# Kernel tuning notes

Measured on AMD Instinct MI355X. Metric: run time of the kernel, lower is better.

The kernel has to match this reference:

```python
import jax, jax.numpy as jnp
import numpy as np

H, NH, HD = 1024, 16, 64
WIN = 256
W = WIN // 2  # one-sided window
EXP = 4
PAD_VAL = 0.0  # pad_token_id
B, S0 = 2, 2048
NEG = float(np.finfo(np.float32).min)


def setup_inputs() -> dict:
    key = jax.random.key(0)
    ks = jax.random.split(key, 12)

    def lin(k, fi, fo):
        k1, k2 = jax.random.split(k)
        w = jax.random.normal(k1, (fi, fo), jnp.float32) / np.float32(np.sqrt(fi))
        b = jax.random.normal(k2, (fo,), jnp.float32) * 0.02
        return w, b

    x = jax.random.normal(ks[0], (B, S0, H), jnp.float32)
    mask = jnp.zeros((B, S0), jnp.int32)  # 0 = real token, 1 = pad
    wq, bq = lin(ks[1], H, H)
    wk, bk = lin(ks[2], H, H)
    wv, bv = lin(ks[3], H, H)
    wqg, bqg = lin(ks[4], H, H)
    wkg, bkg = lin(ks[5], H, H)
    wvg, bvg = lin(ks[6], H, H)
    ln_g = jnp.ones((H,), jnp.float32)
    ln_b = jnp.zeros((H,), jnp.float32)
    w1, b1 = lin(ks[7], H, H * EXP)
    w2, b2 = lin(ks[8], H * EXP, H)
    return dict(x=x, mask=mask, wq=wq, bq=bq, wk=wk, bk=bk, wv=wv, bv=bv,
                wqg=wqg, bqg=bqg, wkg=wkg, bkg=bkg, wvg=wvg, bvg=bvg,
                ln_g=ln_g, ln_b=ln_b, w1=w1, b1=b1, w2=w2, b2=b2)


def _forward(x, mask, wq, bq, wk, bk, wv, bv, wqg, bqg, wkg, bkg, wvg, bvg,
             ln_g, ln_b, w1, b1, w2, b2):
    Bsz, s0, _ = x.shape
    pad = WIN - s0 % WIN
    xp = jnp.pad(x, ((0, 0), (0, pad), (0, 0)), constant_values=PAD_VAL)
    m = jnp.pad(mask, ((0, 0), (0, pad)), constant_values=1)
    S = s0 + pad
    lm = (m * -10000).at[:, -1].set(10000)  # [B,S]; task='cls': last token global
    is_masked = lm < 0
    remove = lm != 0  # masked OR global keys removed from local windows

    inv_sqrt = np.float32(1.0 / np.sqrt(HD))
    q = ((xp @ wq + bq) * inv_sqrt).reshape(Bsz, S, NH, HD)
    k = (xp @ wk + bk).reshape(Bsz, S, NH, HD)
    v = (xp @ wv + bv).reshape(Bsz, S, NH, HD)

    nc = S // W
    # chunked banded scores: query chunk of W attends to 3W keys (prev/self/next)
    qc = q.transpose(0, 2, 1, 3).reshape(Bsz, NH, nc, W, HD)
    kpad = jnp.pad(k.transpose(0, 2, 1, 3), ((0, 0), (0, 0), (W, W), (0, 0)))
    idx3w = jnp.arange(nc)[:, None] * W + jnp.arange(3 * W)[None, :]  # [nc,3W]
    kc = kpad[:, :, idx3w]  # [B,NH,nc,3W,HD]
    sc = jnp.einsum('bhcpd,bhckd->bhcpk', qc, kc)  # [B,NH,nc,W,3W]
    p_idx = jnp.arange(W)[:, None]
    d_idx = jnp.arange(2 * W + 1)[None, :]
    band = sc[:, :, :, p_idx, p_idx + d_idx]  # [B,NH,nc,W,2W+1]
    band = band.reshape(Bsz, NH, S, 2 * W + 1).transpose(0, 2, 1, 3)  # [B,S,NH,2W+1]

    # key index j = i + d - W for offset d in [0, 2W]
    j = jnp.arange(S)[:, None] + jnp.arange(2 * W + 1)[None, :] - W
    in_range = (j >= 0) & (j < S)
    jc = jnp.clip(j, 0, S - 1)
    fmask = jnp.where(remove, NEG, 0.0)  # [B,S]
    band = band + fmask[:, jc][:, :, None, :]
    band = jnp.where(in_range[None, :, None, :], band, -jnp.inf)

    # global key column (single global token = last position), concatenated in front
    gcol = jnp.einsum('bshd,bhd->bsh', q, k[:, -1])[..., None]  # [B,S,NH,1]
    scores = jnp.concatenate([gcol, band], axis=-1)  # [B,S,NH,2W+2]
    probs = jax.nn.softmax(scores, axis=-1)
    probs = jnp.where(is_masked[:, :, None, None], 0.0, probs)

    out_g = probs[..., 0][..., None] * v[:, -1][:, None]  # [B,S,NH,HD]
    lp = probs[..., 1:].transpose(0, 2, 1, 3).reshape(Bsz, NH, nc, W, 2 * W + 1)
    pc = jnp.zeros((Bsz, NH, nc, W, 3 * W), probs.dtype).at[:, :, :, p_idx, p_idx + d_idx].set(lp)
    vpad = jnp.pad(v.transpose(0, 2, 1, 3), ((0, 0), (0, 0), (W, W), (0, 0)))
    vc = vpad[:, :, idx3w]  # [B,NH,nc,3W,HD]
    out_l = jnp.einsum('bhcpk,bhckd->bhcpd', pc, vc).reshape(Bsz, NH, S, HD).transpose(0, 2, 1, 3)
    attn = (out_l + out_g).reshape(Bsz, S, H)

    # full global attention for the global token (separate projections)
    qg = ((xp[:, -1] @ wqg + bqg) * inv_sqrt).reshape(Bsz, NH, HD)
    kg = (xp @ wkg + bkg).reshape(Bsz, S, NH, HD)
    vg = (xp @ wvg + bvg).reshape(Bsz, S, NH, HD)
    gs = jnp.einsum('bhd,bshd->bhs', qg, kg)
    gs = jnp.where(is_masked[:, None, :], NEG, gs)
    gout = jnp.einsum('bhs,bshd->bhd', jax.nn.softmax(gs, axis=-1), vg).reshape(Bsz, H)
    attn = attn.at[:, -1].set(gout)

    y = (xp + attn)[:, :s0]  # residual then strip padding
    mu = y.mean(-1, keepdims=True)
    var = ((y - mu) ** 2).mean(-1, keepdims=True)
    y = (y - mu) * jax.lax.rsqrt(var + 1e-5) * ln_g + ln_b
    h = jax.nn.gelu(y @ w1 + b1, approximate=False)
    return y + (h @ w2 + b2)


def reference(x, mask, wq, bq, wk, bk, wv, bv, wqg, bqg, wkg, bkg, wvg, bvg,
              ln_g, ln_b, w1, b1, w2, b2):
    return _forward(x, mask, wq, bq, wk, bk, wv, bv, wqg, bqg, wkg, bkg,
                    wvg, bvg, ln_g, ln_b, w1, b1, w2, b2)
```

## Files before the change

kernel.cpp:

```cpp
#include <hip/hip_runtime.h>


using bf16x8 = __attribute__((ext_vector_type(8))) short;
using bf16x4 = __attribute__((ext_vector_type(4))) short;
using f32x4  = __attribute__((ext_vector_type(4))) float;

__device__ __forceinline__ float b2f(short s) {
    return __uint_as_float(((unsigned int)(unsigned short)s) << 16);
}
__device__ __forceinline__ short f2b(float f) {
    unsigned int u = __float_as_uint(f);
    u += 0x7fffu + ((u >> 16) & 1u);
    return (short)(u >> 16);
}
__device__ __forceinline__ f32x4 mfma16(bf16x8 a, bf16x8 b, f32x4 c) {
    return __builtin_amdgcn_mfma_f32_16x16x32_bf16(a, b, c, 0, 0, 0);
}
__device__ __forceinline__ float safe_exp(float x) {
    return expf((x <= 0.f) ? x : 0.f);
}
__device__ __forceinline__ void load_lds16(const short* g, short* l) {
    __builtin_amdgcn_global_load_lds((const __attribute__((address_space(1))) void*)g,
                                     (__attribute__((address_space(3))) void*)l, 16, 0, 0);
}
#define NEGF (-3.0e38f)

__global__ void cvt_f32_bf16(const float* __restrict__ in, short* __restrict__ out, int n) {
    int i = (blockIdx.x * 256 + threadIdx.x) * 4;
    f32x4 v = *(const f32x4*)(in + i);
    bf16x4 o;
#pragma unroll
    for (int j = 0; j < 4; ++j) o[j] = f2b(v[j]);
    *(bf16x4*)(out + i) = o;
}

__global__ void cvt_transpose(const float* __restrict__ in, short* __restrict__ out,
                              int R, int C) {
    __shared__ short tile[32][33];
    int bx = blockIdx.x * 32, by = blockIdx.y * 32;
    int tx = threadIdx.x, ty = threadIdx.y;
    for (int i = ty; i < 32; i += 8)
        tile[i][tx] = f2b(in[(size_t)(by + i) * C + bx + tx]);
    __syncthreads();
    for (int i = ty; i < 32; i += 8)
        out[(size_t)(bx + i) * R + by + tx] = tile[tx][i];
}

__global__ void cvt_transpose_qkv(const float* __restrict__ wq, const float* __restrict__ wk,
                                  const float* __restrict__ wv, short* __restrict__ out) {
    __shared__ short tile[32][33];
    const float* in = (blockIdx.z == 0) ? wq : (blockIdx.z == 1) ? wk : wv;
    short* dst = out + (size_t)blockIdx.z * 1024 * 1024;
    int bx = blockIdx.x * 32, by = blockIdx.y * 32;
    int tx = threadIdx.x, ty = threadIdx.y;
    for (int i = ty; i < 32; i += 8)
        tile[i][tx] = f2b(in[(size_t)(by + i) * 1024 + bx + tx]);
    __syncthreads();
    for (int i = ty; i < 32; i += 8)
        dst[(size_t)(bx + i) * 1024 + by + tx] = tile[tx][i];
}

__global__ void transpose_v(const short* __restrict__ QKV, short* __restrict__ Vt) {
    __shared__ short tile[32][33];
    int bh = blockIdx.z; int b = bh >> 4, h = bh & 15;
    int j0 = blockIdx.x * 32, d0 = blockIdx.y * 32;
    int tx = threadIdx.x, ty = threadIdx.y;
    const short* src = QKV + (size_t)b * 2048 * 3072 + 2048 + h * 64;
    for (int i = ty; i < 32; i += 8)
        tile[i][tx] = src[(size_t)(j0 + i) * 3072 + d0 + tx];
    __syncthreads();
    short* dst = Vt + ((size_t)bh * 64 + d0) * 2048 + j0;
    for (int i = ty; i < 32; i += 8)
        dst[(size_t)i * 2048 + tx] = tile[tx][i];
}

__global__ __launch_bounds__(256, 2) void gemm_bt(
    const short* __restrict__ A, const short* __restrict__ Bt,
    const float* __restrict__ bias0, const float* __restrict__ bias1,
    const float* __restrict__ bias2,
    short* __restrict__ C,
    int M, int N, int K, float scale, int scale_cols, int mode)
{
    __shared__ short As[128 * 32];
    __shared__ short Bs[128 * 32];
    int m0 = blockIdx.x * 128, n0 = blockIdx.y * 128;
    int t = threadIdx.x;
    int wave = t >> 6, lane = t & 63, quad = lane >> 4, l16 = lane & 15;
    int wr = (wave >> 1) * 64, wc = (wave & 1) * 64;

    int ch0 = wave * 64 + lane;
    int ch1 = (4 + wave) * 64 + lane;
    int r0 = ch0 >> 2, kc0 = (ch0 & 3) * 8;
    int r1 = ch1 >> 2, kc1 = (ch1 & 3) * 8;
    const short* a0 = A  + (size_t)(m0 + r0) * K + kc0;
    const short* a1 = A  + (size_t)(m0 + r1) * K + kc1;
    const short* b0 = Bt + (size_t)(n0 + r0) * K + kc0;
    const short* b1 = Bt + (size_t)(n0 + r1) * K + kc1;
    short* lA0 = As + wave * 512;
    short* lA1 = As + (4 + wave) * 512;
    short* lB0 = Bs + wave * 512;
    short* lB1 = Bs + (4 + wave) * 512;

    f32x4 acc[4][4] = {};
    for (int k0 = 0; k0 < K; k0 += 32) {
        load_lds16(a0 + k0, lA0);
        load_lds16(a1 + k0, lA1);
        load_lds16(b0 + k0, lB0);
        load_lds16(b1 + k0, lB1);
        __syncthreads();
        bf16x8 af[4], bfr[4];
#pragma unroll
        for (int i = 0; i < 4; ++i)
            af[i] = *(bf16x8*)(As + (wr + i * 16 + l16) * 32 + quad * 8);
#pragma unroll
        for (int j = 0; j < 4; ++j)
            bfr[j] = *(bf16x8*)(Bs + (wc + j * 16 + l16) * 32 + quad * 8);
#pragma unroll
        for (int i = 0; i < 4; ++i)
#pragma unroll
            for (int j = 0; j < 4; ++j)
                acc[i][j] = mfma16(af[i], bfr[j], acc[i][j]);
        __syncthreads();
    }
#pragma unroll
    for (int j = 0; j < 4; ++j) {
        int col = n0 + wc + j * 16 + l16;
        int seg = col >> 10;
        const float* bp = (seg == 0) ? bias0 : (seg == 1) ? bias1 : bias2;
        float bs = bp[col & 1023];
        float sc = (col < scale_cols) ? scale : 1.0f;
#pragma unroll
        for (int i = 0; i < 4; ++i) {
#pragma unroll
            for (int r = 0; r < 4; ++r) {
                int row = m0 + wr + i * 16 + quad * 4 + r;
                float v = acc[i][j][r] + bs;
                if (mode == 0) {
                    C[(size_t)row * N + col] = f2b(v * sc);
                } else {
                    v = 0.5f * v * (1.0f + erff(v * 0.70710678118f));
                    C[(size_t)row * N + col] = f2b(v);
                }
            }
        }
    }
}

__global__ __launch_bounds__(256, 4) void gemm64_bt(
    const short* __restrict__ A, const short* __restrict__ Bt,
    const float* __restrict__ bias, const float* __restrict__ resf,
    float* __restrict__ Cf, int M, int N, int K)
{
    __shared__ short As[64 * 32];
    __shared__ short Bs[64 * 32];
    int m0 = blockIdx.x * 64, n0 = blockIdx.y * 64;
    int t = threadIdx.x;
    int wave = t >> 6, lane = t & 63, quad = lane >> 4, l16 = lane & 15;
    int wr = (wave >> 1) * 32, wc = (wave & 1) * 32;

    int ch = wave * 64 + lane;
    int r0 = ch >> 2, kc0 = (ch & 3) * 8;
    const short* a0 = A  + (size_t)(m0 + r0) * K + kc0;
    const short* b0 = Bt + (size_t)(n0 + r0) * K + kc0;
    short* lA = As + wave * 512;
    short* lB = Bs + wave * 512;

    f32x4 acc[2][2] = {};
    for (int k0 = 0; k0 < K; k0 += 32) {
        load_lds16(a0 + k0, lA);
        load_lds16(b0 + k0, lB);
        __syncthreads();
        bf16x8 af[2], bfr[2];
#pragma unroll
        for (int i = 0; i < 2; ++i)
            af[i] = *(bf16x8*)(As + (wr + i * 16 + l16) * 32 + quad * 8);
#pragma unroll
        for (int j = 0; j < 2; ++j)
            bfr[j] = *(bf16x8*)(Bs + (wc + j * 16 + l16) * 32 + quad * 8);
#pragma unroll
        for (int i = 0; i < 2; ++i)
#pragma unroll
            for (int j = 0; j < 2; ++j)
                acc[i][j] = mfma16(af[i], bfr[j], acc[i][j]);
        __syncthreads();
    }
#pragma unroll
    for (int j = 0; j < 2; ++j) {
        int col = n0 + wc + j * 16 + l16;
        float bs = bias[col];
#pragma unroll
        for (int i = 0; i < 2; ++i) {
#pragma unroll
            for (int r = 0; r < 4; ++r) {
                int row = m0 + wr + i * 16 + quad * 4 + r;
                Cf[(size_t)row * N + col] = acc[i][j][r] + bs + resf[(size_t)row * N + col];
            }
        }
    }
}

__global__ __launch_bounds__(256, 2) void attn_kernel(
    const short* __restrict__ QKV, const short* __restrict__ Vt,
    const int* __restrict__ mask,
    const float* __restrict__ bk, const float* __restrict__ bv,
    short* __restrict__ attn)
{
    extern __shared__ char smem[];
    short* PsQ = (short*)smem;
    short* KV  = (short*)(smem + 34816);
    float* gkf = (float*)(smem + 53248);
    float* gvf = (float*)(smem + 53504);

    int blk = blockIdx.x;
    int c = blk & 15, h = (blk >> 4) & 15, b = blk >> 8;
    int t = threadIdx.x;
    int wave = t >> 6, lane = t & 63, quad = lane >> 4, l16 = lane & 15;
    int q0 = c * 128;
    const int bs_off = b * 2048;
    const short* Q = QKV + h * 64;
    const short* K = QKV + 1024 + h * 64;

#pragma unroll
    for (int l = 0; l < 4; ++l) {
        int idx = l * 256 + t;
        int p = idx >> 3, dc = (idx & 7) * 8;
        *(bf16x8*)(PsQ + p * 72 + dc) =
            *(const bf16x8*)(Q + ((size_t)(bs_off + q0 + p)) * 3072 + dc);
    }
    if (t < 64) { gkf[t] = bk[h * 64 + t]; gvf[t] = bv[h * 64 + t]; }
    __syncthreads();

    bf16x8 aq[2][2];
#pragma unroll
    for (int ti = 0; ti < 2; ++ti)
#pragma unroll
        for (int ks = 0; ks < 2; ++ks)
            aq[ti][ks] = *(bf16x8*)(PsQ + (wave * 32 + ti * 16 + l16) * 72 + ks * 32 + quad * 8);

    float s_g[2][4];
#pragma unroll
    for (int ti = 0; ti < 2; ++ti)
#pragma unroll
        for (int r = 0; r < 4; ++r) {
            int row = wave * 32 + ti * 16 + quad * 4 + r;
            float part = 0.f;
#pragma unroll
            for (int dd = 0; dd < 4; ++dd) {
                int d = l16 * 4 + dd;
                part += b2f(PsQ[row * 72 + d]) * gkf[d];
            }
#pragma unroll
            for (int dsh = 1; dsh < 16; dsh <<= 1) part += __shfl_xor(part, dsh);
            s_g[ti][r] = part;
        }

    f32x4 o_acc[2][4] = {};
    float m_run[2][4], l_run[2][4];
#pragma unroll
    for (int ti = 0; ti < 2; ++ti)
#pragma unroll
        for (int r = 0; r < 4; ++r) { m_run[ti][r] = NEGF; l_run[ti][r] = 0.f; }

    int kt_beg = (q0 == 0) ? 1 : 0;
    int kt_end = (q0 + 256 > 2048) ? 2 : 3;
    for (int kt = kt_beg; kt < kt_end; ++kt) {
        int jb = q0 + (kt - 1) * 128;
        __syncthreads();
#pragma unroll
        for (int l = 0; l < 4; ++l) {
            int idx = l * 256 + t;
            int p = idx >> 3, dc = (idx & 7) * 8;
            *(bf16x8*)(KV + p * 72 + dc) =
                *(const bf16x8*)(K + ((size_t)(bs_off + jb + p)) * 3072 + dc);
        }
        __syncthreads();

        f32x4 s_acc[2][8] = {};
#pragma unroll
        for (int ks = 0; ks < 2; ++ks) {
            bf16x8 bk8[8];
#pragma unroll
            for (int tj = 0; tj < 8; ++tj)
                bk8[tj] = *(bf16x8*)(KV + (tj * 16 + l16) * 72 + ks * 32 + quad * 8);
#pragma unroll
            for (int ti = 0; ti < 2; ++ti)
#pragma unroll
                for (int tj = 0; tj < 8; ++tj)
                    s_acc[ti][tj] = mfma16(aq[ti][ks], bk8[tj], s_acc[ti][tj]);
        }

        float negj[8]; int jcol[8];
#pragma unroll
        for (int tj = 0; tj < 8; ++tj) {
            jcol[tj] = jb + tj * 16 + l16;
            negj[tj] = (mask[bs_off + jcol[tj]] != 0) ? NEGF : 0.f;
        }
        float tmax[2][4];
#pragma unroll
        for (int ti = 0; ti < 2; ++ti)
#pragma unroll
            for (int r = 0; r < 4; ++r) tmax[ti][r] = NEGF;
#pragma unroll
        for (int ti = 0; ti < 2; ++ti) {
            int irow_base = q0 + wave * 32 + ti * 16 + quad * 4;
#pragma unroll
            for (int tj = 0; tj < 8; ++tj)
#pragma unroll
                for (int r = 0; r < 4; ++r) {
                    int dj = jcol[tj] - (irow_base + r);
                    float sc = (dj >= -128 && dj <= 128) ? (s_acc[ti][tj][r] + negj[tj]) : NEGF;
                    s_acc[ti][tj][r] = sc;
                    tmax[ti][r] = fmaxf(tmax[ti][r], sc);
                }
        }
#pragma unroll
        for (int ti = 0; ti < 2; ++ti)
#pragma unroll
            for (int r = 0; r < 4; ++r)
#pragma unroll
                for (int dsh = 1; dsh < 16; dsh <<= 1)
                    tmax[ti][r] = fmaxf(tmax[ti][r], __shfl_xor(tmax[ti][r], dsh));

        float alpha[2][4], lsum[2][4];
#pragma unroll
        for (int ti = 0; ti < 2; ++ti)
#pragma unroll
            for (int r = 0; r < 4; ++r) {
                float mnew = fmaxf(m_run[ti][r], tmax[ti][r]);
                alpha[ti][r] = safe_exp(m_run[ti][r] - mnew);
                m_run[ti][r] = mnew;
                lsum[ti][r] = 0.f;
            }
#pragma unroll
        for (int ti = 0; ti < 2; ++ti)
#pragma unroll
            for (int tj = 0; tj < 8; ++tj)
#pragma unroll
                for (int r = 0; r < 4; ++r) {
                    float p = safe_exp(s_acc[ti][tj][r] - m_run[ti][r]);
                    lsum[ti][r] += p;
                    PsQ[(wave * 32 + ti * 16 + quad * 4 + r) * 136 + tj * 16 + l16] = f2b(p);
                }
#pragma unroll
        for (int ti = 0; ti < 2; ++ti)
#pragma unroll
            for (int r = 0; r < 4; ++r) {
#pragma unroll
                for (int dsh = 1; dsh < 16; dsh <<= 1) lsum[ti][r] += __shfl_xor(lsum[ti][r], dsh);
                l_run[ti][r] = l_run[ti][r] * alpha[ti][r] + lsum[ti][r];
            }
#pragma unroll
        for (int ti = 0; ti < 2; ++ti)
#pragma unroll
            for (int dj = 0; dj < 4; ++dj)
#pragma unroll
                for (int r = 0; r < 4; ++r) o_acc[ti][dj][r] *= alpha[ti][r];

        __syncthreads();
#pragma unroll
        for (int l = 0; l < 4; ++l) {
            int idx = l * 256 + t;
            int d = idx >> 4, kc = (idx & 15) * 8;
            *(bf16x8*)(KV + d * 136 + kc) =
                *(const bf16x8*)(Vt + ((size_t)(b * 16 + h) * 64 + d) * 2048 + jb + kc);
        }
        __syncthreads();
#pragma unroll
        for (int ks = 0; ks < 4; ++ks) {
            bf16x8 ap[2], bv8[4];
#pragma unroll
            for (int ti = 0; ti < 2; ++ti)
                ap[ti] = *(bf16x8*)(PsQ + (wave * 32 + ti * 16 + l16) * 136 + ks * 32 + quad * 8);
#pragma unroll
            for (int dj = 0; dj < 4; ++dj)
                bv8[dj] = *(bf16x8*)(KV + (dj * 16 + l16) * 136 + ks * 32 + quad * 8);
#pragma unroll
            for (int ti = 0; ti < 2; ++ti)
#pragma unroll
                for (int dj = 0; dj < 4; ++dj)
                    o_acc[ti][dj] = mfma16(ap[ti], bv8[dj], o_acc[ti][dj]);
        }
    }

#pragma unroll
    for (int ti = 0; ti < 2; ++ti) {
        int irow_base = q0 + wave * 32 + ti * 16 + quad * 4;
#pragma unroll
        for (int r = 0; r < 4; ++r) {
            int i = irow_base + r;
            float m2 = fmaxf(m_run[ti][r], s_g[ti][r]);
            float pg = safe_exp(s_g[ti][r] - m2);
            float al = safe_exp(m_run[ti][r] - m2);
            float l2 = l_run[ti][r] * al + pg;
            float invl = 1.f / fmaxf(l2, 1e-30f);
            float qm = (mask[bs_off + i] > 0) ? 0.f : 1.f;
#pragma unroll
            for (int dj = 0; dj < 4; ++dj) {
                int d = dj * 16 + l16;
                float val = (o_acc[ti][dj][r] * al + pg * gvf[d]) * invl * qm;
                attn[((size_t)(bs_off + i)) * 1024 + h * 64 + d] = f2b(val);
            }
        }
    }
}

__global__ __launch_bounds__(256) void resid_ln(
    const float* __restrict__ x, const short* __restrict__ attn,
    const float* __restrict__ g, const float* __restrict__ be,
    short* __restrict__ yb, float* __restrict__ yf)
{
    int row = blockIdx.x, t = threadIdx.x;
    int lane = t & 63, wave = t >> 6;
    const size_t base = (size_t)row * 1024;
    float v[4]; float s = 0.f, s2 = 0.f;
#pragma unroll
    for (int i = 0; i < 4; ++i) {
        int c = i * 256 + t;
        float val = x[base + c] + b2f(attn[base + c]);
        v[i] = val; s += val; s2 += val * val;
    }
#pragma unroll
    for (int off = 32; off > 0; off >>= 1) { s += __shfl_xor(s, off); s2 += __shfl_xor(s2, off); }
    __shared__ float red[8];
    if (lane == 0) { red[wave] = s; red[4 + wave] = s2; }
    __syncthreads();
    s  = red[0] + red[1] + red[2] + red[3];
    s2 = red[4] + red[5] + red[6] + red[7];
    float mu  = s * (1.f / 1024.f);
    float var = s2 * (1.f / 1024.f) - mu * mu;
    float inv = rsqrtf(fmaxf(var, 0.f) + 1e-5f);
#pragma unroll
    for (int i = 0; i < 4; ++i) {
        int c = i * 256 + t;
        float o = (v[i] - mu) * inv * g[c] + be[c];
        yb[base + c] = f2b(o);
        yf[base + c] = o;
    }
}

static constexpr size_t MEG      = 1048576;
static constexpr size_t OFF_WQKV = 0;
static constexpr size_t OFF_W1T  = 3 * MEG;
static constexpr size_t OFF_W2T  = 7 * MEG;
static constexpr size_t OFF_XB   = 11 * MEG;
static constexpr size_t OFF_QKV  = 15 * MEG;
static constexpr size_t OFF_VT   = 27 * MEG;
static constexpr size_t OFF_ATT  = 31 * MEG;
static constexpr size_t OFF_YN   = 35 * MEG;
static constexpr size_t OFF_YF   = 39 * MEG;
static constexpr size_t OFF_H    = OFF_QKV;

extern "C" void kernel_launch(void* const* d_in, const int* in_sizes, int n_in,
                              void* d_out, int out_size, void* d_ws, size_t ws_size,
                              hipStream_t stream) {
    (void)in_sizes; (void)n_in; (void)out_size; (void)ws_size;
    const float* x    = (const float*)d_in[0];
    const int*   mask = (const int*)  d_in[1];
    const float* wq   = (const float*)d_in[2];
    const float* bq   = (const float*)d_in[3];
    const float* wk   = (const float*)d_in[4];
    const float* bk   = (const float*)d_in[5];
    const float* wv   = (const float*)d_in[6];
    const float* bv   = (const float*)d_in[7];
    const float* lng  = (const float*)d_in[14];
    const float* lnb  = (const float*)d_in[15];
    const float* w1   = (const float*)d_in[16];
    const float* b1   = (const float*)d_in[17];
    const float* w2   = (const float*)d_in[18];
    const float* b2   = (const float*)d_in[19];
    short* ws  = (short*)d_ws;
    float* out = (float*)d_out;

    dim3 tb(32, 8);
    cvt_transpose_qkv<<<dim3(32, 32, 3), tb, 0, stream>>>(wq, wk, wv, ws + OFF_WQKV);
    cvt_transpose<<<dim3(128, 32), tb, 0, stream>>>(w1, ws + OFF_W1T, 1024, 4096);
    cvt_transpose<<<dim3(32, 128), tb, 0, stream>>>(w2, ws + OFF_W2T, 4096, 1024);
    cvt_f32_bf16<<<4096, 256, 0, stream>>>(x, ws + OFF_XB, 4194304);

    gemm_bt<<<dim3(32, 24), 256, 0, stream>>>(ws + OFF_XB, ws + OFF_WQKV,
                                              bq, bk, bv,
                                              ws + OFF_QKV,
                                              4096, 3072, 1024, 0.125f, 1024, 0);
    transpose_v<<<dim3(64, 2, 32), tb, 0, stream>>>(ws + OFF_QKV, ws + OFF_VT);

    attn_kernel<<<512, 256, 53760, stream>>>(ws + OFF_QKV, ws + OFF_VT,
                                             mask, bk, bv, ws + OFF_ATT);

    resid_ln<<<4096, 256, 0, stream>>>(x, ws + OFF_ATT, lng, lnb,
                                       ws + OFF_YN, (float*)(ws + OFF_YF));

    gemm_bt<<<dim3(32, 32), 256, 0, stream>>>(ws + OFF_YN, ws + OFF_W1T,
                                              b1, b1, b1,
                                              ws + OFF_H,
                                              4096, 4096, 1024, 1.0f, 0, 1);
    gemm64_bt<<<dim3(64, 16), 256, 0, stream>>>(ws + OFF_H, ws + OFF_W2T,
                                                b2, (const float*)(ws + OFF_YF),
                                                out, 4096, 1024, 4096);
}
```

Before: 357.4 us.

## Double GEMM K-tile to 64 with XOR-swizzled LDS and fuse V transpose into QKV epilogue

Both GEMM kernels now stage a 64-wide K slice per iteration instead of 32. Global-to-LDS chunks are XOR-swizzled to avoid bank conflicts, which halves the number of barriers per K sweep. The QKV GEMM epilogue writes the V third directly in transposed [b,h,d,s] layout, removing the separate transpose_v kernel and its extra read/write pass. Occupancy hint rises to 3 blocks while LDS per block doubles, which could limit residency and change register pressure.

```diff
diff --git a/kernel.cpp b/kernel.cpp
--- a/kernel.cpp
+++ b/kernel.cpp
@@ -60,86 +60,95 @@
         dst[(size_t)(bx + i) * 1024 + by + tx] = tile[tx][i];
 }
 
-__global__ void transpose_v(const short* __restrict__ QKV, short* __restrict__ Vt) {
-    __shared__ short tile[32][33];
-    int bh = blockIdx.z; int b = bh >> 4, h = bh & 15;
-    int j0 = blockIdx.x * 32, d0 = blockIdx.y * 32;
-    int tx = threadIdx.x, ty = threadIdx.y;
-    const short* src = QKV + (size_t)b * 2048 * 3072 + 2048 + h * 64;
-    for (int i = ty; i < 32; i += 8)
-        tile[i][tx] = src[(size_t)(j0 + i) * 3072 + d0 + tx];
-    __syncthreads();
-    short* dst = Vt + ((size_t)bh * 64 + d0) * 2048 + j0;
-    for (int i = ty; i < 32; i += 8)
-        dst[(size_t)i * 2048 + tx] = tile[tx][i];
-}
-
-__global__ __launch_bounds__(256, 2) void gemm_bt(
+__global__ __launch_bounds__(256, 3) void gemm_bt(
     const short* __restrict__ A, const short* __restrict__ Bt,
     const float* __restrict__ bias0, const float* __restrict__ bias1,
     const float* __restrict__ bias2,
-    short* __restrict__ C,
-    int M, int N, int K, float scale, int scale_cols, int mode)
+    short* __restrict__ C, short* __restrict__ Vt,
+    int M, int N, int K, float scale, int mode)
 {
-    __shared__ short As[128 * 32];
-    __shared__ short Bs[128 * 32];
+    __shared__ short As[128 * 64];
+    __shared__ short Bs[128 * 64];
     int m0 = blockIdx.x * 128, n0 = blockIdx.y * 128;
     int t = threadIdx.x;
     int wave = t >> 6, lane = t & 63, quad = lane >> 4, l16 = lane & 15;
     int wr = (wave >> 1) * 64, wc = (wave & 1) * 64;
 
-    int ch0 = wave * 64 + lane;
-    int ch1 = (4 + wave) * 64 + lane;
-    int r0 = ch0 >> 2, kc0 = (ch0 & 3) * 8;
-    int r1 = ch1 >> 2, kc1 = (ch1 & 3) * 8;
-    const short* a0 = A  + (size_t)(m0 + r0) * K + kc0;
-    const short* a1 = A  + (size_t)(m0 + r1) * K + kc1;
-    const short* b0 = Bt + (size_t)(n0 + r0) * K + kc0;
-    const short* b1 = Bt + (size_t)(n0 + r1) * K + kc1;
-    short* lA0 = As + wave * 512;
-    short* lA1 = As + (4 + wave) * 512;
-    short* lB0 = Bs + wave * 512;
-    short* lB1 = Bs + (4 + wave) * 512;
+    const short* ap[4]; const short* bp[4]; short* la[4]; short* lb[4];
+    int gk = (((lane & 7) ^ (lane >> 3)) * 8);
+#pragma unroll
+    for (int l = 0; l < 4; ++l) {
+        int c = wave * 4 + l;
+        int row = c * 8 + (lane >> 3);
+        ap[l] = A  + (size_t)(m0 + row) * K + gk;
+        bp[l] = Bt + (size_t)(n0 + row) * K + gk;
+        la[l] = As + c * 512;
+        lb[l] = Bs + c * 512;
+    }
+    int sw = l16 & 7;
 
     f32x4 acc[4][4] = {};
-    for (int k0 = 0; k0 < K; k0 += 32) {
-        load_lds16(a0 + k0, lA0);
-        load_lds16(a1 + k0, lA1);
-        load_lds16(b0 + k0, lB0);
-        load_lds16(b1 + k0, lB1);
-        __syncthreads();
-        bf16x8 af[4], bfr[4];
-#pragma unroll
-        for (int i = 0; i < 4; ++i)
-            af[i] = *(bf16x8*)(As + (wr + i * 16 + l16) * 32 + quad * 8);
-#pragma unroll
-        for (int j = 0; j < 4; ++j)
-            bfr[j] = *(bf16x8*)(Bs + (wc + j * 16 + l16) * 32 + quad * 8);
-#pragma unroll
-        for (int i = 0; i < 4; ++i)
+    for (int k0 = 0; k0 < K; k0 += 64) {
+#pragma unroll
+        for (int l = 0; l < 4; ++l) { load_lds16(ap[l] + k0, la[l]); load_lds16(bp[l] + k0, lb[l]); }
+        __syncthreads();
+#pragma unroll
+        for (int ks = 0; ks < 2; ++ks) {
+            int slot = ((ks * 4 + quad) ^ sw) * 8;
+            bf16x8 af[4], bfr[4];
+#pragma unroll
+            for (int i = 0; i < 4; ++i)
+                af[i] = *(bf16x8*)(As + (wr + i * 16 + l16) * 64 + slot);
 #pragma unroll
             for (int j = 0; j < 4; ++j)
-                acc[i][j] = mfma16(af[i], bfr[j], acc[i][j]);
-        __syncthreads();
-    }
+                bfr[j] = *(bf16x8*)(Bs + (wc + j * 16 + l16) * 64 + slot);
+#pragma unroll
+            for (int i = 0; i < 4; ++i)
+#pragma unroll
+                for (int j = 0; j < 4; ++j)
+                    acc[i][j] = mfma16(af[i], bfr[j], acc[i][j]);
+        }
+        __syncthreads();
+    }
+
 #pragma unroll
     for (int j = 0; j < 4; ++j) {
         int col = n0 + wc + j * 16 + l16;
-        int seg = col >> 10;
-        const float* bp = (seg == 0) ? bias0 : (seg == 1) ? bias1 : bias2;
-        float bs = bp[col & 1023];
-        float sc = (col < scale_cols) ? scale : 1.0f;
-#pragma unroll
-        for (int i = 0; i < 4; ++i) {
-#pragma unroll
-            for (int r = 0; r < 4; ++r) {
-                int row = m0 + wr + i * 16 + quad * 4 + r;
-                float v = acc[i][j][r] + bs;
-                if (mode == 0) {
-                    C[(size_t)row * N + col] = f2b(v * sc);
-                } else {
+        if (mode == 1) {
+            float bs = bias0[col];
+#pragma unroll
+            for (int i = 0; i < 4; ++i) {
+#pragma unroll
+                for (int r = 0; r < 4; ++r) {
+                    int row = m0 + wr + i * 16 + quad * 4 + r;
+                    float v = acc[i][j][r] + bs;
                     v = 0.5f * v * (1.0f + erff(v * 0.70710678118f));
                     C[(size_t)row * N + col] = f2b(v);
+                }
+            }
+        } else {
+            int seg = col >> 10;
+            const float* bpt = (seg == 0) ? bias0 : (seg == 1) ? bias1 : bias2;
+            float bs = bpt[col & 1023];
+            if (seg < 2) {
+                float sc = (seg == 0) ? scale : 1.0f;
+#pragma unroll
+                for (int i = 0; i < 4; ++i)
+#pragma unroll
+                    for (int r = 0; r < 4; ++r) {
+                        int row = m0 + wr + i * 16 + quad * 4 + r;
+                        C[(size_t)row * N + col] = f2b((acc[i][j][r] + bs) * sc);
+                    }
+            } else {
+                int h = (col >> 6) & 15, d = col & 63;
+#pragma unroll
+                for (int i = 0; i < 4; ++i) {
+                    int row0 = m0 + wr + i * 16 + quad * 4;
+                    int bb = row0 >> 11, s0 = row0 & 2047;
+                    bf16x4 vv;
+#pragma unroll
+                    for (int r = 0; r < 4; ++r) vv[r] = f2b(acc[i][j][r] + bs);
+                    *(bf16x4*)(Vt + (((size_t)(bb * 16 + h)) * 64 + d) * 2048 + s0) = vv;
                 }
             }
         }
@@ -151,37 +160,47 @@
     const float* __restrict__ bias, const float* __restrict__ resf,
     float* __restrict__ Cf, int M, int N, int K)
 {
-    __shared__ short As[64 * 32];
-    __shared__ short Bs[64 * 32];
+    __shared__ short As[64 * 64];
+    __shared__ short Bs[64 * 64];
     int m0 = blockIdx.x * 64, n0 = blockIdx.y * 64;
     int t = threadIdx.x;
     int wave = t >> 6, lane = t & 63, quad = lane >> 4, l16 = lane & 15;
     int wr = (wave >> 1) * 32, wc = (wave & 1) * 32;
 
-    int ch = wave * 64 + lane;
-    int r0 = ch >> 2, kc0 = (ch & 3) * 8;
-    const short* a0 = A  + (size_t)(m0 + r0) * K + kc0;
-    const short* b0 = Bt + (size_t)(n0 + r0) * K + kc0;
-    short* lA = As + wave * 512;
-    short* lB = Bs + wave * 512;
+    const short* ap[2]; const short* bp[2]; short* la[2]; short* lb[2];
+    int gk = (((lane & 7) ^ (lane >> 3)) * 8);
+#pragma unroll
+    for (int l = 0; l < 2; ++l) {
+        int c = wave * 2 + l;
+        int row = c * 8 + (lane >> 3);
+        ap[l] = A  + (size_t)(m0 + row) * K + gk;
+        bp[l] = Bt + (size_t)(n0 + row) * K + gk;
+        la[l] = As + c * 512;
+        lb[l] = Bs + c * 512;
+    }
+    int sw = l16 & 7;
 
     f32x4 acc[2][2] = {};
-    for (int k0 = 0; k0 < K; k0 += 32) {
-        load_lds16(a0 + k0, lA);
-        load_lds16(b0 + k0, lB);
-        __syncthreads();
-        bf16x8 af[2], bfr[2];
-#pragma unroll
-        for (int i = 0; i < 2; ++i)
-            af[i] = *(bf16x8*)(As + (wr + i * 16 + l16) * 32 + quad * 8);
-#pragma unroll
-        for (int j = 0; j < 2; ++j)
-            bfr[j] = *(bf16x8*)(Bs + (wc + j * 16 + l16) * 32 + quad * 8);
-#pragma unroll
-        for (int i = 0; i < 2; ++i)
+    for (int k0 = 0; k0 < K; k0 += 64) {
+#pragma unroll
+        for (int l = 0; l < 2; ++l) { load_lds16(ap[l] + k0, la[l]); load_lds16(bp[l] + k0, lb[l]); }
+        __syncthreads();
+#pragma unroll
+        for (int ks = 0; ks < 2; ++ks) {
+            int slot = ((ks * 4 + quad) ^ sw) * 8;
+            bf16x8 af[2], bfr[2];
+#pragma unroll
+            for (int i = 0; i < 2; ++i)
+                af[i] = *(bf16x8*)(As + (wr + i * 16 + l16) * 64 + slot);
 #pragma unroll
             for (int j = 0; j < 2; ++j)
-                acc[i][j] = mfma16(af[i], bfr[j], acc[i][j]);
+                bfr[j] = *(bf16x8*)(Bs + (wc + j * 16 + l16) * 64 + slot);
+#pragma unroll
+            for (int i = 0; i < 2; ++i)
+#pragma unroll
+                for (int j = 0; j < 2; ++j)
+                    acc[i][j] = mfma16(af[i], bfr[j], acc[i][j]);
+        }
         __syncthreads();
     }
 #pragma unroll
@@ -479,9 +498,8 @@
 
     gemm_bt<<<dim3(32, 24), 256, 0, stream>>>(ws + OFF_XB, ws + OFF_WQKV,
                                               bq, bk, bv,
-                                              ws + OFF_QKV,
-                                              4096, 3072, 1024, 0.125f, 1024, 0);
-    transpose_v<<<dim3(64, 2, 32), tb, 0, stream>>>(ws + OFF_QKV, ws + OFF_VT);
+                                              ws + OFF_QKV, ws + OFF_VT,
+                                              4096, 3072, 1024, 0.125f, 0);
 
     attn_kernel<<<512, 256, 53760, stream>>>(ws + OFF_QKV, ws + OFF_VT,
                                              mask, bk, bv, ws + OFF_ATT);
@@ -490,9 +508,9 @@
                                        ws + OFF_YN, (float*)(ws + OFF_YF));
 
     gemm_bt<<<dim3(32, 32), 256, 0, stream>>>(ws + OFF_YN, ws + OFF_W1T,
-                                              b1, b1, b1,
-                                              ws + OFF_H,
-                                              4096, 4096, 1024, 1.0f, 0, 1);
+                                              b1, nullptr, nullptr,
+                                              ws + OFF_H, nullptr,
+                                              4096, 4096, 1024, 1.0f, 1);
     gemm64_bt<<<dim3(64, 16), 256, 0, stream>>>(ws + OFF_H, ws + OFF_W2T,
                                                 b2, (const float*)(ws + OFF_YF),
                                                 out, 4096, 1024, 4096);
```

New measurement: 334.7 us. 6.3% less time.
